# Kernel optimization log

Hardware: AMD Instinct MI355X
Metric: run time of the kernel (lower is better)

The kernel has to match this reference:

```python
import jax, jax.numpy as jnp
import numpy as np

EMBED_DIM = 256
MIN_SCALE = 0.5
BASE = 100.0
NDIM = 3
EPS = 1e-5


def basis_norm(psi, w):
    # w: [B, N] float weights; reduce over token dim (-2)
    norm_sq = jnp.sum(w[..., None] * (psi * psi), axis=-2, keepdims=True)
    return psi / jnp.sqrt(norm_sq + EPS)


def rotary(f, coords, lift):
    # lift: [D//2, 3]; phase: [B, N, D//2]
    phase = coords @ lift.T
    c, s = jnp.cos(phase), jnp.sin(phase)
    f1, f2 = jnp.split(f, 2, axis=-1)
    return jnp.concatenate([f1 * c - f2 * s, f1 * s + f2 * c], axis=-1)


def setup_inputs() -> dict:
    key = jax.random.key(0)
    ks = jax.random.split(key, 12)
    B, N, D = 4, 8192, EMBED_DIM
    phi = jax.random.normal(ks[0], (B, N, D), dtype=jnp.float32)
    coords = jax.random.normal(ks[1], (B, N, NDIM), dtype=jnp.float32)
    weights = jax.random.uniform(ks[2], (B, N), dtype=jnp.float32)
    scale = 1.0 / np.sqrt(D)
    Wq = jax.random.normal(ks[3], (D, D), dtype=jnp.float32) * scale
    bq = jnp.zeros((D,), dtype=jnp.float32)
    Wk = jax.random.normal(ks[4], (D, D), dtype=jnp.float32) * scale
    bk = jax.random.normal(ks[5], (D,), dtype=jnp.float32) * 0.01
    Wv = jax.random.normal(ks[6], (D, D), dtype=jnp.float32) * scale
    bv = jax.random.normal(ks[7], (D,), dtype=jnp.float32) * 0.01
    Wo = jax.random.normal(ks[8], (D, D), dtype=jnp.float32) * scale
    bo = jnp.zeros((D,), dtype=jnp.float32)
    # rotary lift init: k_norms * random unit vecs
    half = D // 2
    scales = BASE ** (-2.0 * np.arange(half) / D)
    k_norms = (2.0 * np.pi / MIN_SCALE) * scales  # [half]
    u = np.asarray(jax.random.normal(ks[9], (half, NDIM)))
    u = u / np.linalg.norm(u, axis=-1, keepdims=True)
    lift = jnp.asarray(k_norms[:, None] * u, dtype=jnp.float32)  # [half, 3]
    return {"phi": phi, "coords": coords, "weights": weights,
            "Wq": Wq, "bq": bq, "Wk": Wk, "bk": bk, "Wv": Wv, "bv": bv,
            "Wo": Wo, "bo": bo, "lift": lift}


def reference(phi, coords, weights, Wq, bq, Wk, bk, Wv, bv, Wo, bo, lift):
    q = phi @ Wq.T + bq
    k = basis_norm(phi @ Wk.T + bk, weights)
    v = basis_norm(phi @ Wv.T + bv, weights)
    q = rotary(q, coords, lift)
    k = rotary(k, coords, lift)
    k = k * weights[..., None]  # float-weights branch
    kv = jnp.einsum('bnd,bne->bde', k, v)   # [B, D, D]
    out = jnp.einsum('bnd,bde->bne', q, kv)  # [B, N, D]
    return out @ Wo.T + bo
```

## Files before the change

kernel.cpp:

```cpp
#include <hip/hip_runtime.h>
#include <hip/hip_bf16.h>
#include <stdint.h>

#define DEV __device__ __forceinline__

typedef short short8 __attribute__((ext_vector_type(8)));
typedef float floatx4 __attribute__((ext_vector_type(4)));
typedef uint32_t uint32x4 __attribute__((ext_vector_type(4)));

constexpr int D = 256;
constexpr int NTOK = 8192;
constexpr int MTOT = 4 * NTOK;

DEV void gl_lds16(const void* g, void* l) {
  __builtin_amdgcn_global_load_lds(
      (const __attribute__((address_space(1))) void*)g,
      (__attribute__((address_space(3))) void*)l, 16, 0, 0);
}

DEV float bflo(uint32_t u) { return __uint_as_float(u << 16); }
DEV float bfhi(uint32_t u) { return __uint_as_float(u & 0xffff0000u); }
DEV uint32_t packbf(float a, float b) {
  uint16_t xa = __builtin_bit_cast(uint16_t, __float2bfloat16(a));
  uint16_t xb = __builtin_bit_cast(uint16_t, __float2bfloat16(b));
  return (uint32_t)xa | ((uint32_t)xb << 16);
}

constexpr int PHI_E = MTOT * D;
constexpr int W_E = D * D;
__global__ __launch_bounds__(256) void convert(
    const float* __restrict__ phi, const float* __restrict__ Wq,
    const float* __restrict__ Wk, const float* __restrict__ Wv,
    uint32_t* __restrict__ dst, float2* __restrict__ nszero) {
  if (blockIdx.x == 0) {
    const float2 z = {0.f, 0.f};
#pragma unroll
    for (int k = 0; k < 4; k++) nszero[k * 256 + threadIdx.x] = z;
  }
  const int idx2 = blockIdx.x * 256 + threadIdx.x;
  const int e0 = idx2 * 2;
  float2 v;
  if (e0 < PHI_E) {
    v = ((const float2*)phi)[idx2];
  } else {
    int r = e0 - PHI_E;
    if (r < W_E) v = ((const float2*)Wq)[r >> 1];
    else if (r < 2 * W_E) v = ((const float2*)Wk)[(r - W_E) >> 1];
    else v = ((const float2*)Wv)[(r - 2 * W_E) >> 1];
  }
  dst[idx2] = packbf(v.x, v.y);
}

__global__ __launch_bounds__(256, 2) void gemm_qkv(
    const __hip_bfloat16* __restrict__ phi,
    const __hip_bfloat16* __restrict__ W16,
    const float* __restrict__ bq, const float* __restrict__ bk, const float* __restrict__ bv,
    const float* __restrict__ coords, const float* __restrict__ wts,
    const float* __restrict__ lift,
    __hip_bfloat16* __restrict__ Qb, __hip_bfloat16* __restrict__ Kb,
    __hip_bfloat16* __restrict__ Vb, float* __restrict__ nsk, float* __restrict__ nsv) {
  __shared__ __align__(16) char As[8192];
  __shared__ __align__(16) char Bs[16384];
  const int t = threadIdx.x, lane = t & 63, wid = t >> 6;
  const int wm = (wid & 1) * 64, wn = (wid >> 1) * 64;
  const int l16 = lane & 15, q4 = lane >> 4;
  const int m0 = blockIdx.x * 128;
  const int mat = blockIdx.y;
  const __hip_bfloat16* W = W16 + (size_t)mat * W_E;
  const float* bias = (mat == 0) ? bq : (mat == 1) ? bk : bv;
  __hip_bfloat16* Out = (mat == 0) ? Qb : (mat == 1) ? Kb : Vb;

  floatx4 acc[4][8] = {};

  const int srow = wid * 16 + (lane >> 2);
  const int skoff = (lane & 3) * 8;
  const __hip_bfloat16* gA = phi + (size_t)(m0 + srow) * D + skoff;
  const __hip_bfloat16* gB = W + (size_t)srow * D + skoff;
  char* lA = As + srow * 64 + skoff * 2;
  char* lB = Bs + srow * 64 + skoff * 2;

  for (int kt = 0; kt < 256; kt += 32) {
    gl_lds16(gA + kt, lA);
    gl_lds16(gA + kt + 64 * D, lA + 4096);
    gl_lds16(gB + kt, lB);
    gl_lds16(gB + kt + 64 * D, lB + 4096);
    gl_lds16(gB + kt + 128 * D, lB + 8192);
    gl_lds16(gB + kt + 192 * D, lB + 12288);
    __syncthreads();
    short8 af[4], bf8[8];
#pragma unroll
    for (int i = 0; i < 4; i++)
      af[i] = *(const short8*)(As + (wm + i * 16 + l16) * 64 + q4 * 16);
#pragma unroll
    for (int j = 0; j < 8; j++) {
      const int col = wn + (j & 3) * 16 + (j >> 2) * 128 + l16;
      bf8[j] = *(const short8*)(Bs + col * 64 + q4 * 16);
    }
#pragma unroll
    for (int i = 0; i < 4; i++)
#pragma unroll
      for (int j = 0; j < 8; j++)
        acc[i][j] = __builtin_amdgcn_mfma_f32_16x16x32_bf16(af[i], bf8[j], acc[i][j], 0, 0, 0);
    __syncthreads();
  }

  float bcol[8];
#pragma unroll
  for (int j = 0; j < 8; j++)
    bcol[j] = bias[wn + (j & 3) * 16 + (j >> 2) * 128 + l16];

  if (mat == 0) {
    float lx[4], ly[4], lz[4];
#pragma unroll
    for (int jj = 0; jj < 4; jj++) {
      const int c = wn + jj * 16 + l16;
      lx[jj] = lift[c * 3 + 0]; ly[jj] = lift[c * 3 + 1]; lz[jj] = lift[c * 3 + 2];
    }
#pragma unroll
    for (int i = 0; i < 4; i++) {
#pragma unroll
      for (int r = 0; r < 4; r++) {
        const int row = m0 + wm + i * 16 + q4 * 4 + r;
        const float cx = coords[row * 3 + 0];
        const float cy = coords[row * 3 + 1];
        const float cz = coords[row * 3 + 2];
#pragma unroll
        for (int jj = 0; jj < 4; jj++) {
          const int c = wn + jj * 16 + l16;
          const float p = cx * lx[jj] + cy * ly[jj] + cz * lz[jj];
          float s, cs;
          __sincosf(p, &s, &cs);
          const float f1 = acc[i][jj][r] + bcol[jj];
          const float f2 = acc[i][jj + 4][r] + bcol[jj + 4];
          Out[(size_t)row * D + c]       = __float2bfloat16(f1 * cs - f2 * s);
          Out[(size_t)row * D + c + 128] = __float2bfloat16(f1 * s + f2 * cs);
        }
      }
    }
  } else {
    const int b = m0 >> 13;
    float* ns = (mat == 1) ? nsk : nsv;
    float colsum[8] = {};
#pragma unroll
    for (int i = 0; i < 4; i++) {
#pragma unroll
      for (int r = 0; r < 4; r++) {
        const int row = m0 + wm + i * 16 + q4 * 4 + r;
        const float w = wts[row];
#pragma unroll
        for (int j = 0; j < 8; j++) {
          const int col = wn + (j & 3) * 16 + (j >> 2) * 128 + l16;
          const float psi = acc[i][j][r] + bcol[j];
          Out[(size_t)row * D + col] = __float2bfloat16(psi);
          colsum[j] += w * psi * psi;
        }
      }
    }
#pragma unroll
    for (int j = 0; j < 8; j++) {
      float s = colsum[j];
      s += __shfl_xor(s, 16);
      s += __shfl_xor(s, 32);
      if (q4 == 0) {
        const int col = wn + (j & 3) * 16 + (j >> 2) * 128 + l16;
        atomicAdd(&ns[b * D + col], s);
      }
    }
  }
}

__global__ __launch_bounds__(256, 2) void vproj_pk(
    const __hip_bfloat16* __restrict__ Vb, const float* __restrict__ Wo,
    const float* __restrict__ nsv, __hip_bfloat16* __restrict__ vproj,
    __hip_bfloat16* __restrict__ Kb, const float* __restrict__ coords,
    const float* __restrict__ wts, const float* __restrict__ lift,
    const float* __restrict__ nsk) {
  __shared__ __align__(16) char As[8192];
  __shared__ __align__(16) char Bs[8192];
  __shared__ __align__(16) float isv[256];
  const int bx = blockIdx.x;
  const int t = threadIdx.x;

  if (bx < 512) {
    const int lane = t & 63, wid = t >> 6;
    const int wm = (wid & 1) * 64, wn = (wid >> 1) * 64;
    const int l16 = lane & 15, q4 = lane >> 4;
    const int m0 = (bx >> 1) * 128, n0 = (bx & 1) * 128;
    const int b = m0 >> 13;
    isv[t] = rsqrtf(nsv[b * D + t] + 1e-5f);
    __syncthreads();
    floatx4 acc[4][4] = {};
    const int srow = wid * 16 + (lane >> 2);
    const int skoff = (lane & 3) * 8;
    const __hip_bfloat16* gA = Vb + (size_t)(m0 + srow) * D + skoff;
    const float* gB0 = Wo + (size_t)(n0 + srow) * D + skoff;
    const float* gB1 = Wo + (size_t)(n0 + srow + 64) * D + skoff;
    char* lA = As + srow * 64 + skoff * 2;
    char* lB = Bs + srow * 64 + skoff * 2;
    for (int kt = 0; kt < 256; kt += 32) {
      gl_lds16(gA + kt, lA);
      gl_lds16(gA + kt + 64 * D, lA + 4096);
      const float4 w0 = *(const float4*)(gB0 + kt);
      const float4 w1 = *(const float4*)(gB0 + kt + 4);
      const float4 w2 = *(const float4*)(gB1 + kt);
      const float4 w3 = *(const float4*)(gB1 + kt + 4);
      const float4 i0 = *(const float4*)(&isv[kt + skoff]);
      const float4 i1 = *(const float4*)(&isv[kt + skoff + 4]);
      uint32x4 p0, p1;
      p0[0] = packbf(w0.x * i0.x, w0.y * i0.y);
      p0[1] = packbf(w0.z * i0.z, w0.w * i0.w);
      p0[2] = packbf(w1.x * i1.x, w1.y * i1.y);
      p0[3] = packbf(w1.z * i1.z, w1.w * i1.w);
      p1[0] = packbf(w2.x * i0.x, w2.y * i0.y);
      p1[1] = packbf(w2.z * i0.z, w2.w * i0.w);
      p1[2] = packbf(w3.x * i1.x, w3.y * i1.y);
      p1[3] = packbf(w3.z * i1.z, w3.w * i1.w);
      *(uint32x4*)lB = p0;
      *(uint32x4*)(lB + 4096) = p1;
      __syncthreads();
      short8 af[4], bf8[4];
#pragma unroll
      for (int i = 0; i < 4; i++) {
        af[i]  = *(const short8*)(As + (wm + i * 16 + l16) * 64 + q4 * 16);
        bf8[i] = *(const short8*)(Bs + (wn + i * 16 + l16) * 64 + q4 * 16);
      }
#pragma unroll
      for (int i = 0; i < 4; i++)
#pragma unroll
        for (int j = 0; j < 4; j++)
          acc[i][j] = __builtin_amdgcn_mfma_f32_16x16x32_bf16(af[i], bf8[j], acc[i][j], 0, 0, 0);
      __syncthreads();
    }
#pragma unroll
    for (int j = 0; j < 4; j++) {
      const int colg = n0 + wn + j * 16 + l16;
#pragma unroll
      for (int i = 0; i < 4; i++) {
        const int rowg = m0 + wm + i * 16 + q4 * 4;
#pragma unroll
        for (int r = 0; r < 4; r++)
          vproj[(size_t)(rowg + r) * D + colg] = __float2bfloat16(acc[i][j][r]);
      }
    }
  } else {
    const int j = t & 63, rloc = t >> 6;
    const int pb = bx - 512;
    const int r0 = pb * 256;
    const int b = r0 >> 13;
    const int j0 = 2 * j, j1 = 2 * j + 1;
    const float lx0 = lift[j0 * 3 + 0], ly0 = lift[j0 * 3 + 1], lz0 = lift[j0 * 3 + 2];
    const float lx1 = lift[j1 * 3 + 0], ly1 = lift[j1 * 3 + 1], lz1 = lift[j1 * 3 + 2];
    const int nb = b * D;
    const float ik0 = rsqrtf(nsk[nb + j0] + 1e-5f);
    const float ik1 = rsqrtf(nsk[nb + j1] + 1e-5f);
    const float ik2 = rsqrtf(nsk[nb + 128 + j0] + 1e-5f);
    const float ik3 = rsqrtf(nsk[nb + 128 + j1] + 1e-5f);
    uint32_t* K32 = (uint32_t*)Kb;
    for (int it = 0; it < 64; it++) {
      const size_t row = (size_t)r0 + it * 4 + rloc;
      const float cx = coords[row * 3 + 0];
      const float cy = coords[row * 3 + 1];
      const float cz = coords[row * 3 + 2];
      const float p0 = cx * lx0 + cy * ly0 + cz * lz0;
      const float p1 = cx * lx1 + cy * ly1 + cz * lz1;
      float s0, c0, s1, c1;
      __sincosf(p0, &s0, &c0);
      __sincosf(p1, &s1, &c1);
      const float w = wts[row];
      const size_t base = row * 128;
      const uint32_t klo = K32[base + j], khi = K32[base + 64 + j];
      const float k1a = bflo(klo) * ik0, k1b = bfhi(klo) * ik1;
      const float k2a = bflo(khi) * ik2, k2b = bfhi(khi) * ik3;
      K32[base + j]      = packbf((k1a * c0 - k2a * s0) * w, (k1b * c1 - k2b * s1) * w);
      K32[base + 64 + j] = packbf((k1a * s0 + k2a * c0) * w, (k1b * s1 + k2b * c1) * w);
    }
  }
}

__global__ __launch_bounds__(256, 2) void gemm_tn(
    const __hip_bfloat16* __restrict__ Vp, const __hip_bfloat16* __restrict__ Kwb,
    __hip_bfloat16* __restrict__ part) {
  __shared__ __align__(16) char Asm[128 * 80];
  __shared__ __align__(16) char Bsm[128 * 80];
  const int t = threadIdx.x, lane = t & 63, wid = t >> 6;
  const int wm = (wid & 1) * 64, wn = (wid >> 1) * 64;
  const int l16 = lane & 15, q4 = lane >> 4;
  const int chunk = blockIdx.x, ed = blockIdx.y, b = blockIdx.z;
  const int e0 = (ed & 1) * 128, d0 = (ed >> 1) * 128;
  const uint32_t* V32 = (const uint32_t*)Vp;
  const uint32_t* K32 = (const uint32_t*)Kwb;
  const int s_np = (((t & 3) | ((t >> 6) << 2)) ^ ((t >> 4) & 3));
  const int s_e2lo = (t >> 2) & 15;
  floatx4 acc[4][4] = {};
  for (int nt = 0; nt < 256; nt += 32) {
    const int nbase = chunk * 256 + nt;
    const size_t tokbase = ((size_t)b * NTOK + nbase + 2 * s_np) * 128;
#pragma unroll
    for (int r = 0; r < 4; r++) {
      const int e2 = s_e2lo + r * 16;
      {
        const uint32_t a0 = V32[tokbase + (e0 >> 1) + e2];
        const uint32_t a1 = V32[tokbase + 128 + (e0 >> 1) + e2];
        *(uint32_t*)(Asm + (2 * e2) * 80 + 4 * s_np)     = (a0 & 0xffffu) | (a1 << 16);
        *(uint32_t*)(Asm + (2 * e2 + 1) * 80 + 4 * s_np) = (a0 >> 16) | (a1 & 0xffff0000u);
      }
      {
        const uint32_t b0 = K32[tokbase + (d0 >> 1) + e2];
        const uint32_t b1 = K32[tokbase + 128 + (d0 >> 1) + e2];
        *(uint32_t*)(Bsm + (2 * e2) * 80 + 4 * s_np)     = (b0 & 0xffffu) | (b1 << 16);
        *(uint32_t*)(Bsm + (2 * e2 + 1) * 80 + 4 * s_np) = (b0 >> 16) | (b1 & 0xffff0000u);
      }
    }
    __syncthreads();
    short8 af[4], bf8[4];
#pragma unroll
    for (int i = 0; i < 4; i++) {
      af[i]  = *(const short8*)(Asm + (wm + i * 16 + l16) * 80 + q4 * 16);
      bf8[i] = *(const short8*)(Bsm + (wn + i * 16 + l16) * 80 + q4 * 16);
    }
#pragma unroll
    for (int i = 0; i < 4; i++)
#pragma unroll
      for (int j = 0; j < 4; j++)
        acc[i][j] = __builtin_amdgcn_mfma_f32_16x16x32_bf16(af[i], bf8[j], acc[i][j], 0, 0, 0);
    __syncthreads();
  }
  __hip_bfloat16* pt = part + (((size_t)(chunk * 4 + b)) << 16);
#pragma unroll
  for (int i = 0; i < 4; i++) {
#pragma unroll
    for (int r = 0; r < 4; r++) {
      const int eg = e0 + wm + i * 16 + q4 * 4 + r;
#pragma unroll
      for (int j = 0; j < 4; j++) {
        const int dg = d0 + wn + j * 16 + l16;
        pt[eg * 256 + dg] = __float2bfloat16(acc[i][j][r]);
      }
    }
  }
}

__global__ __launch_bounds__(256) void reduce_kvt(const uint32_t* __restrict__ part,
                                                  uint32_t* __restrict__ P) {
  const int flat2 = blockIdx.x * 256 + threadIdx.x;
  const int b = flat2 >> 15;
  const int off = flat2 & 32767;
  float sx = 0, sy = 0;
#pragma unroll
  for (int c = 0; c < 32; c++) {
    const uint32_t u = part[(((size_t)(c * 4 + b)) << 15) + off];
    sx += bflo(u); sy += bfhi(u);
  }
  P[flat2] = packbf(sx, sy);
}

__global__ __launch_bounds__(256, 2) void gemm_out(
    const __hip_bfloat16* __restrict__ A, const __hip_bfloat16* __restrict__ Pm,
    const float* __restrict__ bo, float* __restrict__ Og) {
  __shared__ __align__(16) char As[8192];
  __shared__ __align__(16) char Bs[8192];
  const int t = threadIdx.x, lane = t & 63, wid = t >> 6;
  const int wm = (wid & 1) * 64, wn = (wid >> 1) * 64;
  const int l16 = lane & 15, q4 = lane >> 4;
  const int m0 = blockIdx.x * 128, n0 = blockIdx.y * 128;
  const int b = m0 >> 13;
  const __hip_bfloat16* W = Pm + ((size_t)b << 16);
  floatx4 acc[4][4] = {};
  const int srow = wid * 16 + (lane >> 2);
  const int skoff = (lane & 3) * 8;
  const __hip_bfloat16* gA = A + (size_t)(m0 + srow) * D + skoff;
  const __hip_bfloat16* gB = W + (size_t)(n0 + srow) * D + skoff;
  char* lA = As + srow * 64 + skoff * 2;
  char* lB = Bs + srow * 64 + skoff * 2;
  for (int kt = 0; kt < 256; kt += 32) {
    gl_lds16(gA + kt, lA);
    gl_lds16(gA + kt + 64 * D, lA + 4096);
    gl_lds16(gB + kt, lB);
    gl_lds16(gB + kt + 64 * D, lB + 4096);
    __syncthreads();
    short8 af[4], bf8[4];
#pragma unroll
    for (int i = 0; i < 4; i++) {
      af[i]  = *(const short8*)(As + (wm + i * 16 + l16) * 64 + q4 * 16);
      bf8[i] = *(const short8*)(Bs + (wn + i * 16 + l16) * 64 + q4 * 16);
    }
#pragma unroll
    for (int i = 0; i < 4; i++)
#pragma unroll
      for (int j = 0; j < 4; j++)
        acc[i][j] = __builtin_amdgcn_mfma_f32_16x16x32_bf16(af[i], bf8[j], acc[i][j], 0, 0, 0);
    __syncthreads();
  }
#pragma unroll
  for (int j = 0; j < 4; j++) {
    const int colg = n0 + wn + j * 16 + l16;
    const float bb = bo[colg];
#pragma unroll
    for (int i = 0; i < 4; i++) {
      const int rowg = m0 + wm + i * 16 + q4 * 4;
#pragma unroll
      for (int r = 0; r < 4; r++)
        Og[(size_t)(rowg + r) * D + colg] = acc[i][j][r] + bb;
    }
  }
}

extern "C" void kernel_launch(void* const* d_in, const int* in_sizes, int n_in,
                              void* d_out, int out_size, void* d_ws, size_t ws_size,
                              hipStream_t stream) {
  const float* phi    = (const float*)d_in[0];
  const float* coords = (const float*)d_in[1];
  const float* wts    = (const float*)d_in[2];
  const float* bq     = (const float*)d_in[4];
  const float* bk     = (const float*)d_in[6];
  const float* bv     = (const float*)d_in[8];
  const float* Wo     = (const float*)d_in[9];
  const float* bo     = (const float*)d_in[10];
  const float* lift   = (const float*)d_in[11];

  char* ws = (char*)d_ws;
  __hip_bfloat16* phi16 = (__hip_bfloat16*)ws;
  __hip_bfloat16* W16   = (__hip_bfloat16*)(ws + 16777216);
  const size_t QOFF = 17170432;
  const size_t SZ = (size_t)MTOT * D * 2;
  __hip_bfloat16* Qb = (__hip_bfloat16*)(ws + QOFF);
  __hip_bfloat16* Kb = (__hip_bfloat16*)(ws + QOFF + SZ);
  __hip_bfloat16* Vb = (__hip_bfloat16*)(ws + QOFF + 2 * SZ);
  const size_t NOFF = QOFF + 3 * SZ;
  float* nsk = (float*)(ws + NOFF);
  float* nsv = (float*)(ws + NOFF + 4096);
  __hip_bfloat16* part = (__hip_bfloat16*)(ws + NOFF + 8192);
  __hip_bfloat16* P = (__hip_bfloat16*)(ws + NOFF + 8192 + 16777216);
  __hip_bfloat16* vproj = (__hip_bfloat16*)(ws + NOFF + 8192 + 16777216 + 524288);

  convert<<<16768, 256, 0, stream>>>(phi, (const float*)d_in[3], (const float*)d_in[5],
                                     (const float*)d_in[7], (uint32_t*)ws, (float2*)(ws + NOFF));
  gemm_qkv<<<dim3(256, 3), 256, 0, stream>>>(phi16, W16, bq, bk, bv, coords, wts, lift,
                                             Qb, Kb, Vb, nsk, nsv);
  vproj_pk<<<640, 256, 0, stream>>>(Vb, Wo, nsv, vproj, Kb, coords, wts, lift, nsk);
  gemm_tn<<<dim3(32, 4, 4), 256, 0, stream>>>(vproj, Kb, part);
  reduce_kvt<<<512, 256, 0, stream>>>((const uint32_t*)part, (uint32_t*)P);
  gemm_out<<<dim3(256, 2), 256, 0, stream>>>(Qb, P, bo, (float*)d_out);
}
```

Before: 191.0 us.

## Fuse fp32-to-bf16 conversion into QKV GEMM and replace atomics with partial norms

Drops the separate convert kernel: gemm_qkv now loads fp32 phi and weights directly, packs them to bf16 in registers and writes to LDS, instead of using direct global-to-LDS loads of pre-converted data. The column norm-square atomics are replaced by per-block partial sums written to a buffer, which the consumer kernel reduces (128 partials per column) before rsqrt. The grid is reordered so the three matrices sharing one phi tile are adjacent blocks, which should improve L2 reuse of the fp32 phi reads. This removes a full pass writing and reading bf16 phi and the zeroing step, at the cost of reading phi in fp32 three times, synchronous loads with no async LDS path, and extra reduction work in vproj_pk.

```diff
diff --git a/kernel.cpp b/kernel.cpp
--- a/kernel.cpp
+++ b/kernel.cpp
@@ -11,6 +11,7 @@
 constexpr int D = 256;
 constexpr int NTOK = 8192;
 constexpr int MTOT = 4 * NTOK;
+constexpr int W_E = D * D;
 
 DEV void gl_lds16(const void* g, void* l) {
   __builtin_amdgcn_global_load_lds(
@@ -26,47 +27,22 @@
   return (uint32_t)xa | ((uint32_t)xb << 16);
 }
 
-constexpr int PHI_E = MTOT * D;
-constexpr int W_E = D * D;
-__global__ __launch_bounds__(256) void convert(
+__global__ __launch_bounds__(256, 2) void gemm_qkv(
     const float* __restrict__ phi, const float* __restrict__ Wq,
     const float* __restrict__ Wk, const float* __restrict__ Wv,
-    uint32_t* __restrict__ dst, float2* __restrict__ nszero) {
-  if (blockIdx.x == 0) {
-    const float2 z = {0.f, 0.f};
-#pragma unroll
-    for (int k = 0; k < 4; k++) nszero[k * 256 + threadIdx.x] = z;
-  }
-  const int idx2 = blockIdx.x * 256 + threadIdx.x;
-  const int e0 = idx2 * 2;
-  float2 v;
-  if (e0 < PHI_E) {
-    v = ((const float2*)phi)[idx2];
-  } else {
-    int r = e0 - PHI_E;
-    if (r < W_E) v = ((const float2*)Wq)[r >> 1];
-    else if (r < 2 * W_E) v = ((const float2*)Wk)[(r - W_E) >> 1];
-    else v = ((const float2*)Wv)[(r - 2 * W_E) >> 1];
-  }
-  dst[idx2] = packbf(v.x, v.y);
-}
-
-__global__ __launch_bounds__(256, 2) void gemm_qkv(
-    const __hip_bfloat16* __restrict__ phi,
-    const __hip_bfloat16* __restrict__ W16,
     const float* __restrict__ bq, const float* __restrict__ bk, const float* __restrict__ bv,
     const float* __restrict__ coords, const float* __restrict__ wts,
     const float* __restrict__ lift,
     __hip_bfloat16* __restrict__ Qb, __hip_bfloat16* __restrict__ Kb,
-    __hip_bfloat16* __restrict__ Vb, float* __restrict__ nsk, float* __restrict__ nsv) {
+    __hip_bfloat16* __restrict__ Vb, float* __restrict__ ns_part) {
   __shared__ __align__(16) char As[8192];
   __shared__ __align__(16) char Bs[16384];
   const int t = threadIdx.x, lane = t & 63, wid = t >> 6;
   const int wm = (wid & 1) * 64, wn = (wid >> 1) * 64;
   const int l16 = lane & 15, q4 = lane >> 4;
-  const int m0 = blockIdx.x * 128;
-  const int mat = blockIdx.y;
-  const __hip_bfloat16* W = W16 + (size_t)mat * W_E;
+  const int mat = blockIdx.x;
+  const int m0 = blockIdx.y * 128;
+  const float* Wsel = (mat == 0) ? Wq : (mat == 1) ? Wk : Wv;
   const float* bias = (mat == 0) ? bq : (mat == 1) ? bk : bv;
   __hip_bfloat16* Out = (mat == 0) ? Qb : (mat == 1) ? Kb : Vb;
 
@@ -74,18 +50,43 @@
 
   const int srow = wid * 16 + (lane >> 2);
   const int skoff = (lane & 3) * 8;
-  const __hip_bfloat16* gA = phi + (size_t)(m0 + srow) * D + skoff;
-  const __hip_bfloat16* gB = W + (size_t)srow * D + skoff;
+  const float* pa = phi + (size_t)(m0 + srow) * D + skoff;
+  const float* pw = Wsel + (size_t)srow * D + skoff;
   char* lA = As + srow * 64 + skoff * 2;
   char* lB = Bs + srow * 64 + skoff * 2;
 
   for (int kt = 0; kt < 256; kt += 32) {
-    gl_lds16(gA + kt, lA);
-    gl_lds16(gA + kt + 64 * D, lA + 4096);
-    gl_lds16(gB + kt, lB);
-    gl_lds16(gB + kt + 64 * D, lB + 4096);
-    gl_lds16(gB + kt + 128 * D, lB + 8192);
-    gl_lds16(gB + kt + 192 * D, lB + 12288);
+    const float4 a0 = *(const float4*)(pa + kt);
+    const float4 a1 = *(const float4*)(pa + kt + 4);
+    const float4 a2 = *(const float4*)(pa + kt + 64 * D);
+    const float4 a3 = *(const float4*)(pa + kt + 64 * D + 4);
+    const float4 w0 = *(const float4*)(pw + kt);
+    const float4 w1 = *(const float4*)(pw + kt + 4);
+    const float4 w2 = *(const float4*)(pw + kt + 64 * D);
+    const float4 w3 = *(const float4*)(pw + kt + 64 * D + 4);
+    const float4 w4 = *(const float4*)(pw + kt + 128 * D);
+    const float4 w5 = *(const float4*)(pw + kt + 128 * D + 4);
+    const float4 w6 = *(const float4*)(pw + kt + 192 * D);
+    const float4 w7 = *(const float4*)(pw + kt + 192 * D + 4);
+    uint32x4 uA0, uA1, uB0, uB1, uB2, uB3;
+    uA0[0] = packbf(a0.x, a0.y); uA0[1] = packbf(a0.z, a0.w);
+    uA0[2] = packbf(a1.x, a1.y); uA0[3] = packbf(a1.z, a1.w);
+    uA1[0] = packbf(a2.x, a2.y); uA1[1] = packbf(a2.z, a2.w);
+    uA1[2] = packbf(a3.x, a3.y); uA1[3] = packbf(a3.z, a3.w);
+    uB0[0] = packbf(w0.x, w0.y); uB0[1] = packbf(w0.z, w0.w);
+    uB0[2] = packbf(w1.x, w1.y); uB0[3] = packbf(w1.z, w1.w);
+    uB1[0] = packbf(w2.x, w2.y); uB1[1] = packbf(w2.z, w2.w);
+    uB1[2] = packbf(w3.x, w3.y); uB1[3] = packbf(w3.z, w3.w);
+    uB2[0] = packbf(w4.x, w4.y); uB2[1] = packbf(w4.z, w4.w);
+    uB2[2] = packbf(w5.x, w5.y); uB2[3] = packbf(w5.z, w5.w);
+    uB3[0] = packbf(w6.x, w6.y); uB3[1] = packbf(w6.z, w6.w);
+    uB3[2] = packbf(w7.x, w7.y); uB3[3] = packbf(w7.z, w7.w);
+    *(uint32x4*)lA = uA0;
+    *(uint32x4*)(lA + 4096) = uA1;
+    *(uint32x4*)lB = uB0;
+    *(uint32x4*)(lB + 4096) = uB1;
+    *(uint32x4*)(lB + 8192) = uB2;
+    *(uint32x4*)(lB + 12288) = uB3;
     __syncthreads();
     short8 af[4], bf8[8];
 #pragma unroll
@@ -112,9 +113,9 @@
   if (mat == 0) {
     float lx[4], ly[4], lz[4];
 #pragma unroll
-    for (int jj = 0; jj < 4; jj++) {
-      const int c = wn + jj * 16 + l16;
-      lx[jj] = lift[c * 3 + 0]; ly[jj] = lift[c * 3 + 1]; lz[jj] = lift[c * 3 + 2];
+    for (int c4 = 0; c4 < 4; c4++) {
+      const int c = wn + c4 * 16 + l16;
+      lx[c4] = lift[c * 3 + 0]; ly[c4] = lift[c * 3 + 1]; lz[c4] = lift[c * 3 + 2];
     }
 #pragma unroll
     for (int i = 0; i < 4; i++) {
@@ -125,13 +126,13 @@
         const float cy = coords[row * 3 + 1];
         const float cz = coords[row * 3 + 2];
 #pragma unroll
-        for (int jj = 0; jj < 4; jj++) {
-          const int c = wn + jj * 16 + l16;
-          const float p = cx * lx[jj] + cy * ly[jj] + cz * lz[jj];
+        for (int c4 = 0; c4 < 4; c4++) {
+          const int c = wn + c4 * 16 + l16;
+          const float p = cx * lx[c4] + cy * ly[c4] + cz * lz[c4];
           float s, cs;
           __sincosf(p, &s, &cs);
-          const float f1 = acc[i][jj][r] + bcol[jj];
-          const float f2 = acc[i][jj + 4][r] + bcol[jj + 4];
+          const float f1 = acc[i][c4][r] + bcol[c4];
+          const float f2 = acc[i][c4 + 4][r] + bcol[c4 + 4];
           Out[(size_t)row * D + c]       = __float2bfloat16(f1 * cs - f2 * s);
           Out[(size_t)row * D + c + 128] = __float2bfloat16(f1 * s + f2 * cs);
         }
@@ -139,7 +140,8 @@
     }
   } else {
     const int b = m0 >> 13;
-    float* ns = (mat == 1) ? nsk : nsv;
+    const int mb2 = ((blockIdx.y & 63) << 1) | (wid & 1);
+    float* ns = ns_part + (((size_t)(mat - 1) * 4 + b) * 128 + mb2) * 256;
     float colsum[8] = {};
 #pragma unroll
     for (int i = 0; i < 4; i++) {
@@ -163,7 +165,7 @@
       s += __shfl_xor(s, 32);
       if (q4 == 0) {
         const int col = wn + (j & 3) * 16 + (j >> 2) * 128 + l16;
-        atomicAdd(&ns[b * D + col], s);
+        ns[col] = s;
       }
     }
   }
@@ -171,23 +173,28 @@
 
 __global__ __launch_bounds__(256, 2) void vproj_pk(
     const __hip_bfloat16* __restrict__ Vb, const float* __restrict__ Wo,
-    const float* __restrict__ nsv, __hip_bfloat16* __restrict__ vproj,
+    const float* __restrict__ ns_part, __hip_bfloat16* __restrict__ vproj,
     __hip_bfloat16* __restrict__ Kb, const float* __restrict__ coords,
-    const float* __restrict__ wts, const float* __restrict__ lift,
-    const float* __restrict__ nsk) {
-  __shared__ __align__(16) char As[8192];
-  __shared__ __align__(16) char Bs[8192];
-  __shared__ __align__(16) float isv[256];
+    const float* __restrict__ wts, const float* __restrict__ lift) {
+  __shared__ __align__(16) char smem[17408];
   const int bx = blockIdx.x;
   const int t = threadIdx.x;
 
   if (bx < 512) {
+    char* As = smem;
+    char* Bs = smem + 8192;
+    float* isv = (float*)(smem + 16384);
     const int lane = t & 63, wid = t >> 6;
     const int wm = (wid & 1) * 64, wn = (wid >> 1) * 64;
     const int l16 = lane & 15, q4 = lane >> 4;
     const int m0 = (bx >> 1) * 128, n0 = (bx & 1) * 128;
     const int b = m0 >> 13;
-    isv[t] = rsqrtf(nsv[b * D + t] + 1e-5f);
+    {
+      const float* np = ns_part + ((size_t)(4 + b) * 128) * 256;
+      float s = 1e-5f;
+      for (int r = 0; r < 128; r++) s += np[r * 256 + t];
+      isv[t] = rsqrtf(s);
+    }
     __syncthreads();
     floatx4 acc[4][4] = {};
     const int srow = wid * 16 + (lane >> 2);
@@ -243,18 +250,23 @@
       }
     }
   } else {
-    const int j = t & 63, rloc = t >> 6;
+    float* snk = (float*)smem;
     const int pb = bx - 512;
     const int r0 = pb * 256;
     const int b = r0 >> 13;
+    {
+      const float* np = ns_part + ((size_t)(0 + b) * 128) * 256;
+      float s = 1e-5f;
+      for (int r = 0; r < 128; r++) s += np[r * 256 + t];
+      snk[t] = rsqrtf(s);
+    }
+    __syncthreads();
+    const int j = t & 63, rloc = t >> 6;
     const int j0 = 2 * j, j1 = 2 * j + 1;
     const float lx0 = lift[j0 * 3 + 0], ly0 = lift[j0 * 3 + 1], lz0 = lift[j0 * 3 + 2];
     const float lx1 = lift[j1 * 3 + 0], ly1 = lift[j1 * 3 + 1], lz1 = lift[j1 * 3 + 2];
-    const int nb = b * D;
-    const float ik0 = rsqrtf(nsk[nb + j0] + 1e-5f);
-    const float ik1 = rsqrtf(nsk[nb + j1] + 1e-5f);
-    const float ik2 = rsqrtf(nsk[nb + 128 + j0] + 1e-5f);
-    const float ik3 = rsqrtf(nsk[nb + 128 + j1] + 1e-5f);
+    const float ik0 = snk[j0], ik1 = snk[j1];
+    const float ik2 = snk[128 + j0], ik3 = snk[128 + j1];
     uint32_t* K32 = (uint32_t*)Kb;
     for (int it = 0; it < 64; it++) {
       const size_t row = (size_t)r0 + it * 4 + rloc;
@@ -411,34 +423,30 @@
   const float* phi    = (const float*)d_in[0];
   const float* coords = (const float*)d_in[1];
   const float* wts    = (const float*)d_in[2];
+  const float* Wq     = (const float*)d_in[3];
   const float* bq     = (const float*)d_in[4];
+  const float* Wk     = (const float*)d_in[5];
   const float* bk     = (const float*)d_in[6];
+  const float* Wv     = (const float*)d_in[7];
   const float* bv     = (const float*)d_in[8];
   const float* Wo     = (const float*)d_in[9];
   const float* bo     = (const float*)d_in[10];
   const float* lift   = (const float*)d_in[11];
 
   char* ws = (char*)d_ws;
-  __hip_bfloat16* phi16 = (__hip_bfloat16*)ws;
-  __hip_bfloat16* W16   = (__hip_bfloat16*)(ws + 16777216);
-  const size_t QOFF = 17170432;
   const size_t SZ = (size_t)MTOT * D * 2;
-  __hip_bfloat16* Qb = (__hip_bfloat16*)(ws + QOFF);
-  __hip_bfloat16* Kb = (__hip_bfloat16*)(ws + QOFF + SZ);
-  __hip_bfloat16* Vb = (__hip_bfloat16*)(ws + QOFF + 2 * SZ);
-  const size_t NOFF = QOFF + 3 * SZ;
-  float* nsk = (float*)(ws + NOFF);
-  float* nsv = (float*)(ws + NOFF + 4096);
-  __hip_bfloat16* part = (__hip_bfloat16*)(ws + NOFF + 8192);
-  __hip_bfloat16* P = (__hip_bfloat16*)(ws + NOFF + 8192 + 16777216);
-  __hip_bfloat16* vproj = (__hip_bfloat16*)(ws + NOFF + 8192 + 16777216 + 524288);
-
-  convert<<<16768, 256, 0, stream>>>(phi, (const float*)d_in[3], (const float*)d_in[5],
-                                     (const float*)d_in[7], (uint32_t*)ws, (float2*)(ws + NOFF));
-  gemm_qkv<<<dim3(256, 3), 256, 0, stream>>>(phi16, W16, bq, bk, bv, coords, wts, lift,
-                                             Qb, Kb, Vb, nsk, nsv);
-  vproj_pk<<<640, 256, 0, stream>>>(Vb, Wo, nsv, vproj, Kb, coords, wts, lift, nsk);
+  __hip_bfloat16* Qb = (__hip_bfloat16*)ws;
+  __hip_bfloat16* Kb = (__hip_bfloat16*)(ws + SZ);
+  __hip_bfloat16* Vb = (__hip_bfloat16*)(ws + 2 * SZ);
+  float* ns_part = (float*)(ws + 3 * SZ);
+  __hip_bfloat16* part  = (__hip_bfloat16*)(ws + 3 * SZ + 1048576);
+  __hip_bfloat16* Pm    = (__hip_bfloat16*)(ws + 4 * SZ + 1048576);
+  __hip_bfloat16* vproj = (__hip_bfloat16*)(ws + 4 * SZ + 1048576 + 524288);
+
+  gemm_qkv<<<dim3(3, 256), 256, 0, stream>>>(phi, Wq, Wk, Wv, bq, bk, bv, coords, wts, lift,
+                                             Qb, Kb, Vb, ns_part);
+  vproj_pk<<<640, 256, 0, stream>>>(Vb, Wo, ns_part, vproj, Kb, coords, wts, lift);
   gemm_tn<<<dim3(32, 4, 4), 256, 0, stream>>>(vproj, Kb, part);
-  reduce_kvt<<<512, 256, 0, stream>>>((const uint32_t*)part, (uint32_t*)P);
-  gemm_out<<<dim3(256, 2), 256, 0, stream>>>(Qb, P, bo, (float*)d_out);
-}
+  reduce_kvt<<<512, 256, 0, stream>>>((const uint32_t*)part, (uint32_t*)Pm);
+  gemm_out<<<dim3(256, 2), 256, 0, stream>>>(Qb, Pm, bo, (float*)d_out);
+}
```

New measurement: 193.9 us. About the same (+1.5%).
